# Performance work log

Measured on AMD Instinct MI355X. Metric: run time of the kernel, lower is better.

The kernel has to match this reference:

```python
import jax, jax.numpy as jnp
import numpy as np

DIM = 96; NH = 3; HD = DIM // NH; SCALE = HD ** -0.5
WS = (7, 7, 7); N = WS[0] * WS[1] * WS[2]
SHIFT = (3, 3, 3)  # half window
NL = 2
GRID = (28, 28, 28)
B = 2


def _rel_index():
    wd, wh, ww = WS
    coords = np.stack(np.meshgrid(np.arange(wd), np.arange(wh), np.arange(ww), indexing='ij')).reshape(3, -1)
    rel = (coords[:, :, None] - coords[:, None, :]).transpose(1, 2, 0)  # [N,N,3]
    rel[..., 0] += wd - 1; rel[..., 1] += wh - 1; rel[..., 2] += ww - 1
    rel[..., 0] *= (2 * wh - 1) * (2 * ww - 1); rel[..., 1] *= (2 * ww - 1)
    return rel.sum(-1)  # [N,N]

REL_IDX = _rel_index()


def _window_partition(x):
    b, D, H, W, C = x.shape
    wd, wh, ww = WS
    x = x.reshape(b, D // wd, wd, H // wh, wh, W // ww, ww, C)
    x = x.transpose(0, 1, 3, 5, 2, 4, 6, 7)
    return x.reshape(-1, N, C)


def _window_reverse(win, b, D, H, W):
    wd, wh, ww = WS
    C = win.shape[-1]
    x = win.reshape(b, D // wd, H // wh, W // ww, wd, wh, ww, C)
    x = x.transpose(0, 1, 4, 2, 5, 3, 6, 7)
    return x.reshape(b, D, H, W, C)


def _compute_mask():
    # MONAI compute_mask for the shifted (SW-MSA) block
    D, H, W = GRID; wd, wh, ww = WS; sd, sh, sw = SHIFT
    img = np.zeros((1, D, H, W, 1), np.float32)
    cnt = 0
    for d in (slice(-wd), slice(-wd, -sd), slice(-sd, None)):
        for h in (slice(-wh), slice(-wh, -sh), slice(-sh, None)):
            for w in (slice(-ww), slice(-ww, -sw), slice(-sw, None)):
                img[:, d, h, w, :] = cnt; cnt += 1
    mw = img.reshape(1, D // wd, wd, H // wh, wh, W // ww, ww, 1)
    mw = mw.transpose(0, 1, 3, 5, 2, 4, 6, 7).reshape(-1, N)  # [nw, N]
    am = mw[:, None, :] - mw[:, :, None]
    return np.where(am != 0, np.float32(-100.0), np.float32(0.0))

MASK = jnp.asarray(_compute_mask())  # [nw, N, N]


def _ln(x, g, b):
    mu = x.mean(-1, keepdims=True)
    var = ((x - mu) ** 2).mean(-1, keepdims=True)
    return (x - mu) / jnp.sqrt(var + 1e-5) * g + b


def _block(x, p, shift, mask):
    b, D, H, W, C = x.shape
    h = _ln(x, p['n1g'], p['n1b'])
    if shift is not None:
        h = jnp.roll(h, (-shift[0], -shift[1], -shift[2]), axis=(1, 2, 3))
    xw = _window_partition(h)  # [b*nw, N, C]
    Bn = xw.shape[0]
    qkv = (xw @ p['qkvw'].T + p['qkvb']).reshape(Bn, N, 3, NH, HD).transpose(2, 0, 3, 1, 4)
    q, k, v = qkv[0] * SCALE, qkv[1], qkv[2]
    attn = jnp.einsum('bhnd,bhmd->bhnm', q, k)
    bias = p['rel'][REL_IDX.reshape(-1)].reshape(N, N, NH).transpose(2, 0, 1)
    attn = attn + bias[None]
    if mask is not None:
        nw = mask.shape[0]
        attn = (attn.reshape(Bn // nw, nw, NH, N, N) + mask[None, :, None]).reshape(Bn, NH, N, N)
    attn = jax.nn.softmax(attn, axis=-1)
    out = jnp.einsum('bhnm,bhmd->bhnd', attn, v).transpose(0, 2, 1, 3).reshape(Bn, N, C)
    out = out @ p['projw'].T + p['projb']
    h = _window_reverse(out, b, D, H, W)
    if shift is not None:
        h = jnp.roll(h, shift, axis=(1, 2, 3))
    x = x + h
    m = _ln(x, p['n2g'], p['n2b'])
    m = jax.nn.gelu(m @ p['fc1w'].T + p['fc1b'], approximate=False) @ p['fc2w'].T + p['fc2b']
    return x + m


def setup_inputs() -> dict:
    key = jax.random.key(0)
    ks = jax.random.split(key, 8)
    nbias = (2 * WS[0] - 1) * (2 * WS[1] - 1) * (2 * WS[2] - 1)
    return {
        'x': jax.random.normal(ks[0], (B,) + GRID + (DIM,), jnp.float32),
        'norm1_g': jnp.ones((NL, DIM), jnp.float32),
        'norm1_b': jnp.zeros((NL, DIM), jnp.float32),
        'qkv_w': jax.random.normal(ks[1], (NL, 3 * DIM, DIM), jnp.float32) * 0.02,
        'qkv_b': jnp.zeros((NL, 3 * DIM), jnp.float32),
        'rel_bias': jax.random.normal(ks[2], (NL, nbias, NH), jnp.float32) * 0.02,
        'proj_w': jax.random.normal(ks[3], (NL, DIM, DIM), jnp.float32) * 0.02,
        'proj_b': jnp.zeros((NL, DIM), jnp.float32),
        'norm2_g': jnp.ones((NL, DIM), jnp.float32),
        'norm2_b': jnp.zeros((NL, DIM), jnp.float32),
        'fc1_w': jax.random.normal(ks[4], (NL, 4 * DIM, DIM), jnp.float32) * 0.02,
        'fc1_b': jnp.zeros((NL, 4 * DIM), jnp.float32),
        'fc2_w': jax.random.normal(ks[5], (NL, DIM, 4 * DIM), jnp.float32) * 0.02,
        'fc2_b': jnp.zeros((NL, DIM), jnp.float32),
    }


def reference(x, norm1_g, norm1_b, qkv_w, qkv_b, rel_bias, proj_w, proj_b,
              norm2_g, norm2_b, fc1_w, fc1_b, fc2_w, fc2_b):
    for i in range(NL):
        p = dict(n1g=norm1_g[i], n1b=norm1_b[i], qkvw=qkv_w[i], qkvb=qkv_b[i],
                 rel=rel_bias[i], projw=proj_w[i], projb=proj_b[i],
                 n2g=norm2_g[i], n2b=norm2_b[i], fc1w=fc1_w[i], fc1b=fc1_b[i],
                 fc2w=fc2_w[i], fc2b=fc2_b[i])
        if i % 2 == 0:
            x = _block(x, p, None, None)  # W-MSA (mask is all-zero for shift=0)
        else:
            x = _block(x, p, SHIFT, MASK)  # SW-MSA
    return x
```

## Files before the change

kernel.cpp:

```cpp
#include <hip/hip_runtime.h>
#include <math.h>

#define DIM 96
#define NHD 3
#define HD 32
#define NWT 343
#define NWIN 128
#define TOK 43904
#define NBIAS 2197
#define SCALE 0.17677669529663687f
#define TPAD 352
#define QTS 5632
#define HSZ (22 * QTS)

typedef __attribute__((ext_vector_type(8))) short bf16x8;
typedef __attribute__((ext_vector_type(4))) float f32x4;

__device__ __forceinline__ unsigned short f2b(float f) {
    union { float f; unsigned int u; } x; x.f = f;
    unsigned int r = (x.u + 0x7fffu + ((x.u >> 16) & 1u)) >> 16;
    return (unsigned short)r;
}
__device__ __forceinline__ unsigned int pk2bf(float a, float b) {
    union { float f; unsigned int u; } x, y; x.f = a; y.f = b;
    return ((x.u + 0x8000u) >> 16) | ((y.u + 0x8000u) & 0xffff0000u);
}
__device__ __forceinline__ float lo16(unsigned int u) {
    union { unsigned int u; float f; } x; x.u = u << 16; return x.f;
}
__device__ __forceinline__ float hi16(unsigned int u) {
    union { unsigned int u; float f; } x; x.u = u & 0xffff0000u; return x.f;
}

__global__ void __launch_bounds__(256) k_cvt4(
        const float* __restrict__ s0, const float* __restrict__ s1,
        const float* __restrict__ s2, const float* __restrict__ s3,
        unsigned short* __restrict__ dst) {
    int i = blockIdx.x * 256 + threadIdx.x;
    if (i >= 221184) return;
    const float* src; int off;
    if (i < 55296)       { src = s0; off = i; }
    else if (i < 73728)  { src = s1; off = i - 55296; }
    else if (i < 147456) { src = s2; off = i - 73728; }
    else                 { src = s3; off = i - 147456; }
    dst[i] = f2b(src[off]);
}

__global__ void __launch_bounds__(256) k_bias(
        const float* __restrict__ rel0, const float* __restrict__ rel1,
        unsigned short* __restrict__ bt) {
    int i = blockIdx.x * 256 + threadIdx.x;
    if (i >= 27 * HSZ) return;
    int off = i % QTS;
    int t = i / QTS;
    int qt = t % 22; t /= 22;
    int head = t % 3; int combo = t / 3;
    int j = off & 7, q4i = (off >> 3) & 3, lm = (off >> 5) & 15, pr = off >> 9;
    int q = min(qt * 16 + lm, 342);
    int kcol = pr * 32 + ((j >> 2) << 4) + q4i * 4 + (j & 3);
    float outv;
    if (kcol >= 343) {
        outv = -100000.0f;
    } else {
        int dq = q / 49, hq = (q / 7) % 7, wq = q % 7;
        int dk = kcol / 49, hk = (kcol / 7) % 7, wk = kcol % 7;
        int ridx = (dq - dk + 6) * 169 + (hq - hk + 6) * 13 + (wq - wk + 6);
        const float* rel = (combo == 0) ? rel0 : rel1;
        float b = rel[ridx * 3 + head];
        if (combo > 0) {
            int ty = combo - 1;
            int rqd = (ty & 4) ? 1 + (dq >= 4) : 0;
            int rqh = (ty & 2) ? 1 + (hq >= 4) : 0;
            int rqw = (ty & 1) ? 1 + (wq >= 4) : 0;
            int rkd = (ty & 4) ? 1 + (dk >= 4) : 0;
            int rkh = (ty & 2) ? 1 + (hk >= 4) : 0;
            int rkw = (ty & 1) ? 1 + (wk >= 4) : 0;
            if (rqd != rkd || rqh != rkh || rqw != rkw) b -= 100.0f;
        }
        outv = b;
    }
    bt[i] = f2b(outv);
}

__global__ void __launch_bounds__(256) k_qkv(
        const float* __restrict__ x, const float* __restrict__ g1,
        const float* __restrict__ b1, const unsigned short* __restrict__ W,
        const float* __restrict__ bias, unsigned short* __restrict__ q,
        unsigned short* __restrict__ k, unsigned short* __restrict__ v, int shift) {
    __shared__ __align__(16) unsigned short lns[64][104];
    __shared__ __align__(16) unsigned short wbuf[96][104];
    int wid = threadIdx.x >> 6, lane = threadIdx.x & 63;
    int lm = lane & 15, q4 = lane >> 4;
    int m0 = blockIdx.x * 64 + wid * 16;
    int bwr[4], nnr[4];
    size_t rowoff[4];
    #pragma unroll
    for (int r = 0; r < 4; ++r) {
        int wtok = m0 + q4 * 4 + r;
        int bw = wtok / NWT, n = wtok % NWT;
        bwr[r] = bw; nnr[r] = n;
        int b = bw >> 6, win = bw & 63;
        int wdi = win >> 4, whi = (win >> 2) & 3, wwi = win & 3;
        int d = n / 49, h = (n / 7) % 7, w = n % 7;
        int sd = (wdi * 7 + d + shift) % 28;
        int sh = (whi * 7 + h + shift) % 28;
        int sw = (wwi * 7 + w + shift) % 28;
        rowoff[r] = (((size_t)(b * 28 + sd) * 28 + sh) * 28 + sw) * 96;
    }
    float val[6][4], g1v[6], b1v[6];
    #pragma unroll
    for (int c = 0; c < 6; ++c) {
        int ncol = c * 16 + lm;
        g1v[c] = g1[ncol]; b1v[c] = b1[ncol];
        #pragma unroll
        for (int r = 0; r < 4; ++r) val[c][r] = x[rowoff[r] + ncol];
    }
    #pragma unroll
    for (int r = 0; r < 4; ++r) {
        float s = 0.f, s2 = 0.f;
        #pragma unroll
        for (int c = 0; c < 6; ++c) { s += val[c][r]; s2 += val[c][r] * val[c][r]; }
        #pragma unroll
        for (int off = 8; off > 0; off >>= 1) {
            s  += __shfl_xor(s,  off, 64);
            s2 += __shfl_xor(s2, off, 64);
        }
        float mu = s * (1.0f / 96.0f);
        float rstd = rsqrtf(s2 * (1.0f / 96.0f) - mu * mu + 1e-5f);
        int row = wid * 16 + q4 * 4 + r;
        #pragma unroll
        for (int c = 0; c < 6; ++c)
            lns[row][c * 16 + lm] = f2b((val[c][r] - mu) * rstd * g1v[c] + b1v[c]);
    }
    __syncthreads();
    bf16x8 a1[3];
    #pragma unroll
    for (int ks = 0; ks < 3; ++ks)
        a1[ks] = *((const bf16x8*)&lns[wid * 16 + lm][ks * 32 + q4 * 8]);
    for (int ch = 0; ch < 3; ++ch) {
        __syncthreads();
        const uint4* src = (const uint4*)(W + ch * 96 * 96);
        for (int s = threadIdx.x; s < 1152; s += 256) {
            int row = s / 12, seg = s % 12;
            *((uint4*)&wbuf[row][seg * 8]) = src[s];
        }
        __syncthreads();
        f32x4 acc[6];
        #pragma unroll
        for (int c = 0; c < 6; ++c) acc[c] = (f32x4){0.f, 0.f, 0.f, 0.f};
        #pragma unroll
        for (int ks = 0; ks < 3; ++ks) {
            #pragma unroll
            for (int c = 0; c < 6; ++c) {
                bf16x8 b = *((const bf16x8*)&wbuf[c * 16 + lm][ks * 32 + q4 * 8]);
                acc[c] = __builtin_amdgcn_mfma_f32_16x16x32_bf16(a1[ks], b, acc[c], 0, 0, 0);
            }
        }
        #pragma unroll
        for (int c = 0; c < 6; ++c) {
            int col = c * 16 + lm;
            int head = col >> 5, hd = col & 31;
            float bb = bias[ch * 96 + col];
            #pragma unroll
            for (int r = 0; r < 4; ++r) {
                int wh = bwr[r] * NHD + head;
                float vv = acc[c][r] + bb;
                if (ch == 0)
                    q[(size_t)wh * (TPAD * 32) + nnr[r] * 32 + hd] = f2b(vv * SCALE);
                else if (ch == 1)
                    k[(size_t)wh * (TPAD * 32) + nnr[r] * 32 + hd] = f2b(vv);
                else
                    v[(size_t)wh * (32 * TPAD) + hd * TPAD + nnr[r]] = f2b(vv);
            }
        }
    }
}

__global__ void __launch_bounds__(256) k_attn(
        const unsigned short* __restrict__ q, const unsigned short* __restrict__ k,
        const unsigned short* __restrict__ vT, const unsigned short* __restrict__ bt,
        unsigned short* __restrict__ o, int tmul) {
    __shared__ __align__(16) unsigned short vts[32 * 360];
    __shared__ __align__(16) unsigned short pbuf[4][2][16 * 40];
    int wh = blockIdx.x / 3, third = blockIdx.x % 3;
    int bw = wh / NHD, head = wh % NHD;
    const unsigned int* vsrc = (const unsigned int*)(vT + (size_t)wh * 32 * TPAD);
    unsigned int* vdst = (unsigned int*)vts;
    for (int i = threadIdx.x; i < 32 * 176; i += 256) {
        int row = i / 176, cc = i - row * 176;
        vdst[row * 180 + cc] = vsrc[i];
    }
    __syncthreads();
    int win = bw & 63;
    int wdi = win >> 4, whi = (win >> 2) & 3, wwi = win & 3;
    int type = ((wdi == 3) ? 4 : 0) | ((whi == 3) ? 2 : 0) | ((wwi == 3) ? 1 : 0);
    const unsigned short* bbase = bt + (size_t)type * tmul + (size_t)head * HSZ;
    int wid = threadIdx.x >> 6, lane = threadIdx.x & 63;
    int lm = lane & 15, q4 = lane >> 4;
    int tb = third * 8 + wid * 2;
    if (tb > 21) return;
    bool dual = (tb + 1 <= 21);
    int qtA = tb, qtB = dual ? tb + 1 : tb;
    const unsigned short* qbase = q + (size_t)wh * TPAD * 32;
    const unsigned short* kbase = k + (size_t)wh * TPAD * 32;
    int qtokA = qtA * 16 + lm, qtokB = qtB * 16 + lm;
    bf16x8 qfA = *((const bf16x8*)(qbase + qtokA * 32 + q4 * 8));
    bf16x8 qfB = *((const bf16x8*)(qbase + qtokB * 32 + q4 * 8));
    const unsigned short* bpA = bbase + (size_t)qtA * QTS + lm * 32 + q4 * 8;
    const unsigned short* bpB = bbase + (size_t)qtB * QTS + lm * 32 + q4 * 8;
    f32x4 aA0 = (f32x4){0.f,0.f,0.f,0.f}, aA1 = aA0, aB0 = aA0, aB1 = aA0;
    float dA = 0.f, dB = 0.f;
    unsigned short* pbA = pbuf[wid][0];
    unsigned short* pbB = pbuf[wid][1];
    bf16x8 kf0n = *((const bf16x8*)(kbase + lm * 32 + q4 * 8));
    bf16x8 kf1n = *((const bf16x8*)(kbase + (16 + lm) * 32 + q4 * 8));
    uint4 bAn = *((const uint4*)bpA);
    uint4 bBn = *((const uint4*)bpB);
    for (int pr = 0; pr < 11; ++pr) {
        int kb0 = pr * 32;
        bf16x8 kf0 = kf0n, kf1 = kf1n;
        uint4 uA = bAn, uB = bBn;
        if (pr < 10) {
            int kb1 = kb0 + 32;
            kf0n = *((const bf16x8*)(kbase + (kb1 + lm) * 32 + q4 * 8));
            kf1n = *((const bf16x8*)(kbase + (kb1 + 16 + lm) * 32 + q4 * 8));
            bAn = *((const uint4*)(bpA + (pr + 1) * 512));
            bBn = *((const uint4*)(bpB + (pr + 1) * 512));
        }
        f32x4 z = (f32x4){0.f, 0.f, 0.f, 0.f};
        f32x4 sA0 = __builtin_amdgcn_mfma_f32_16x16x32_bf16(kf0, qfA, z, 0, 0, 0);
        f32x4 sA1 = __builtin_amdgcn_mfma_f32_16x16x32_bf16(kf1, qfA, z, 0, 0, 0);
        f32x4 sB0 = __builtin_amdgcn_mfma_f32_16x16x32_bf16(kf0, qfB, z, 0, 0, 0);
        f32x4 sB1 = __builtin_amdgcn_mfma_f32_16x16x32_bf16(kf1, qfB, z, 0, 0, 0);
        float pA[8], pB[8];
        pA[0] = __expf(sA0[0] + lo16(uA.x)); pA[1] = __expf(sA0[1] + hi16(uA.x));
        pA[2] = __expf(sA0[2] + lo16(uA.y)); pA[3] = __expf(sA0[3] + hi16(uA.y));
        pA[4] = __expf(sA1[0] + lo16(uA.z)); pA[5] = __expf(sA1[1] + hi16(uA.z));
        pA[6] = __expf(sA1[2] + lo16(uA.w)); pA[7] = __expf(sA1[3] + hi16(uA.w));
        pB[0] = __expf(sB0[0] + lo16(uB.x)); pB[1] = __expf(sB0[1] + hi16(uB.x));
        pB[2] = __expf(sB0[2] + lo16(uB.y)); pB[3] = __expf(sB0[3] + hi16(uB.y));
        pB[4] = __expf(sB1[0] + lo16(uB.z)); pB[5] = __expf(sB1[1] + hi16(uB.z));
        pB[6] = __expf(sB1[2] + lo16(uB.w)); pB[7] = __expf(sB1[3] + hi16(uB.w));
        #pragma unroll
        for (int j = 0; j < 8; ++j) { dA += pA[j]; dB += pB[j]; }
        #pragma unroll
        for (int t = 0; t < 2; ++t) {
            *((unsigned int*)(pbA + lm * 40 + t * 16 + q4 * 4)) =
                pk2bf(pA[t * 4 + 0], pA[t * 4 + 1]);
            *((unsigned int*)(pbA + lm * 40 + t * 16 + q4 * 4 + 2)) =
                pk2bf(pA[t * 4 + 2], pA[t * 4 + 3]);
            *((unsigned int*)(pbB + lm * 40 + t * 16 + q4 * 4)) =
                pk2bf(pB[t * 4 + 0], pB[t * 4 + 1]);
            *((unsigned int*)(pbB + lm * 40 + t * 16 + q4 * 4 + 2)) =
                pk2bf(pB[t * 4 + 2], pB[t * 4 + 3]);
        }
        bf16x8 pfA = *((const bf16x8*)(pbA + lm * 40 + q4 * 8));
        bf16x8 pfB = *((const bf16x8*)(pbB + lm * 40 + q4 * 8));
        bf16x8 v0 = *((const bf16x8*)(vts + lm * 360 + kb0 + q4 * 8));
        bf16x8 v1 = *((const bf16x8*)(vts + (16 + lm) * 360 + kb0 + q4 * 8));
        aA0 = __builtin_amdgcn_mfma_f32_16x16x32_bf16(pfA, v0, aA0, 0, 0, 0);
        aA1 = __builtin_amdgcn_mfma_f32_16x16x32_bf16(pfA, v1, aA1, 0, 0, 0);
        aB0 = __builtin_amdgcn_mfma_f32_16x16x32_bf16(pfB, v0, aB0, 0, 0, 0);
        aB1 = __builtin_amdgcn_mfma_f32_16x16x32_bf16(pfB, v1, aB1, 0, 0, 0);
    }
    dA += __shfl_xor(dA, 16, 64); dA += __shfl_xor(dA, 32, 64);
    dB += __shfl_xor(dB, 16, 64); dB += __shfl_xor(dB, 32, 64);
    #pragma unroll
    for (int r = 0; r < 4; ++r) {
        int qrowA = qtA * 16 + q4 * 4 + r;
        if (qrowA < NWT) {
            float inv = 1.0f / __shfl(dA, q4 * 4 + r, 64);
            unsigned short* op = o + (size_t)(bw * NWT + qrowA) * DIM + head * HD;
            op[lm]      = f2b(aA0[r] * inv);
            op[16 + lm] = f2b(aA1[r] * inv);
        }
    }
    if (dual) {
        #pragma unroll
        for (int r = 0; r < 4; ++r) {
            int qrowB = qtB * 16 + q4 * 4 + r;
            if (qrowB < NWT) {
                float inv = 1.0f / __shfl(dB, q4 * 4 + r, 64);
                unsigned short* op = o + (size_t)(bw * NWT + qrowB) * DIM + head * HD;
                op[lm]      = f2b(aB0[r] * inv);
                op[16 + lm] = f2b(aB1[r] * inv);
            }
        }
    }
}

__global__ void __launch_bounds__(256) k_pm(
        const unsigned short* __restrict__ ao, const unsigned short* __restrict__ Wp,
        const float* __restrict__ pbias, const float* __restrict__ xin,
        float* __restrict__ xout,
        const float* __restrict__ g2, const float* __restrict__ b2,
        const unsigned short* __restrict__ w1, const float* __restrict__ bb1,
        const unsigned short* __restrict__ w2, const float* __restrict__ bb2,
        int shift) {
    __shared__ __align__(16) unsigned short lns[64][104];
    __shared__ __align__(16) unsigned short big[18816];
    int wid = threadIdx.x >> 6, lane = threadIdx.x & 63;
    int lm = lane & 15, q4 = lane >> 4;
    int m0 = blockIdx.x * 64 + wid * 16;
    for (int s = threadIdx.x; s < 1152; s += 256) {
        int row = s / 12, seg = s % 12;
        *((uint4*)&big[row * 104 + seg * 8]) = ((const uint4*)Wp)[s];
    }
    const unsigned short* arow = ao + (size_t)(m0 + lm) * 96;
    bf16x8 a1[3];
    #pragma unroll
    for (int ks = 0; ks < 3; ++ks)
        a1[ks] = *((const bf16x8*)(arow + ks * 32 + q4 * 8));
    __syncthreads();
    f32x4 acc[6];
    #pragma unroll
    for (int c = 0; c < 6; ++c) acc[c] = (f32x4){0.f, 0.f, 0.f, 0.f};
    #pragma unroll
    for (int ks = 0; ks < 3; ++ks) {
        #pragma unroll
        for (int c = 0; c < 6; ++c) {
            bf16x8 b = *((const bf16x8*)&big[(c * 16 + lm) * 104 + ks * 32 + q4 * 8]);
            acc[c] = __builtin_amdgcn_mfma_f32_16x16x32_bf16(a1[ks], b, acc[c], 0, 0, 0);
        }
    }
    size_t rowoff[4];
    #pragma unroll
    for (int r = 0; r < 4; ++r) {
        int wtok = m0 + q4 * 4 + r;
        int bw = wtok / NWT, n = wtok % NWT;
        int b = bw >> 6, win = bw & 63;
        int wdi = win >> 4, whi = (win >> 2) & 3, wwi = win & 3;
        int d = n / 49, h = (n / 7) % 7, w = n % 7;
        int sd = (wdi * 7 + d + shift) % 28;
        int sh = (whi * 7 + h + shift) % 28;
        int sw = (wwi * 7 + w + shift) % 28;
        rowoff[r] = (((size_t)(b * 28 + sd) * 28 + sh) * 28 + sw) * 96;
    }
    float val[6][4], g2v[6], b2v[6];
    #pragma unroll
    for (int c = 0; c < 6; ++c) {
        int n = c * 16 + lm;
        float bb = pbias[n];
        g2v[c] = g2[n]; b2v[c] = b2[n];
        #pragma unroll
        for (int r = 0; r < 4; ++r)
            val[c][r] = xin[rowoff[r] + n] + acc[c][r] + bb;
    }
    #pragma unroll
    for (int r = 0; r < 4; ++r) {
        float s = 0.f, s2 = 0.f;
        #pragma unroll
        for (int c = 0; c < 6; ++c) { s += val[c][r]; s2 += val[c][r] * val[c][r]; }
        #pragma unroll
        for (int off = 8; off > 0; off >>= 1) {
            s  += __shfl_xor(s,  off, 64);
            s2 += __shfl_xor(s2, off, 64);
        }
        float mu = s * (1.0f / 96.0f);
        float rstd = rsqrtf(s2 * (1.0f / 96.0f) - mu * mu + 1e-5f);
        int row = wid * 16 + q4 * 4 + r;
        #pragma unroll
        for (int c = 0; c < 6; ++c)
            lns[row][c * 16 + lm] = f2b((val[c][r] - mu) * rstd * g2v[c] + b2v[c]);
    }
    bf16x8 am[3];
    #pragma unroll
    for (int ks = 0; ks < 3; ++ks)
        am[ks] = *((const bf16x8*)&lns[wid * 16 + lm][ks * 32 + q4 * 8]);
    f32x4 acc2[6];
    #pragma unroll
    for (int c = 0; c < 6; ++c) acc2[c] = (f32x4){0.f, 0.f, 0.f, 0.f};
    unsigned short* hid_ = &big[13952 + wid * 1216];
    for (int ch = 0; ch < 6; ++ch) {
        __syncthreads();
        const uint4* src1 = (const uint4*)(w1 + ch * 64 * 96);
        #pragma unroll
        for (int t = 0; t < 3; ++t) {
            int s = threadIdx.x + t * 256;
            int row = s / 12, seg = s % 12;
            *((uint4*)&big[row * 104 + seg * 8]) = src1[s];
        }
        #pragma unroll
        for (int t = 0; t < 3; ++t) {
            int s = threadIdx.x + t * 256;
            int row = s >> 3, seg = s & 7;
            *((uint4*)&big[6656 + row * 76 + seg * 8]) =
                *((const uint4*)(w2 + row * 384 + ch * 64 + seg * 8));
        }
        __syncthreads();
        f32x4 acc1[4];
        #pragma unroll
        for (int t = 0; t < 4; ++t) acc1[t] = (f32x4){0.f, 0.f, 0.f, 0.f};
        #pragma unroll
        for (int ks = 0; ks < 3; ++ks) {
            #pragma unroll
            for (int t = 0; t < 4; ++t) {
                bf16x8 b = *((const bf16x8*)&big[(t * 16 + lm) * 104 + ks * 32 + q4 * 8]);
                acc1[t] = __builtin_amdgcn_mfma_f32_16x16x32_bf16(am[ks], b, acc1[t], 0, 0, 0);
            }
        }
        #pragma unroll
        for (int t = 0; t < 4; ++t) {
            float bb = bb1[ch * 64 + t * 16 + lm];
            #pragma unroll
            for (int r = 0; r < 4; ++r) {
                float v2 = acc1[t][r] + bb;
                float t2 = v2 * v2;
                float m = fmaf(-0.0713548162f, t2, -1.5957691216f);
                float e = __expf(v2 * m);
                float ge = v2 * (1.0f / (1.0f + e));
                hid_[(q4 * 4 + r) * 76 + t * 16 + lm] = f2b(ge);
            }
        }
        #pragma unroll
        for (int ks2 = 0; ks2 < 2; ++ks2) {
            bf16x8 a = *((const bf16x8*)(hid_ + lm * 76 + ks2 * 32 + q4 * 8));
            #pragma unroll
            for (int c = 0; c < 6; ++c) {
                bf16x8 b = *((const bf16x8*)&big[6656 + (c * 16 + lm) * 76 + ks2 * 32 + q4 * 8]);
                acc2[c] = __builtin_amdgcn_mfma_f32_16x16x32_bf16(a, b, acc2[c], 0, 0, 0);
            }
        }
    }
    #pragma unroll
    for (int c = 0; c < 6; ++c) {
        int n = c * 16 + lm;
        float bb = bb2[n];
        #pragma unroll
        for (int r = 0; r < 4; ++r)
            xout[rowoff[r] + n] = val[c][r] + acc2[c][r] + bb;
    }
}

extern "C" void kernel_launch(void* const* d_in, const int* in_sizes, int n_in,
                              void* d_out, int out_size, void* d_ws, size_t ws_size,
                              hipStream_t stream) {
    const float* x     = (const float*)d_in[0];
    const float* n1g   = (const float*)d_in[1];
    const float* n1b   = (const float*)d_in[2];
    const float* qkvw  = (const float*)d_in[3];
    const float* qkvb  = (const float*)d_in[4];
    const float* relb  = (const float*)d_in[5];
    const float* projw = (const float*)d_in[6];
    const float* projb = (const float*)d_in[7];
    const float* n2g   = (const float*)d_in[8];
    const float* n2b   = (const float*)d_in[9];
    const float* fc1w  = (const float*)d_in[10];
    const float* fc1b  = (const float*)d_in[11];
    const float* fc2w  = (const float*)d_in[12];
    const float* fc2b  = (const float*)d_in[13];
    float* out = (float*)d_out;

    const size_t NEL = (size_t)TOK * DIM;
    const size_t QKN = (size_t)NWIN * NHD * TPAD * 32;
    float* buf_x = (float*)d_ws;
    unsigned short* hbuf = (unsigned short*)(buf_x + NEL);
    unsigned short* bq   = hbuf + NEL;
    unsigned short* bk   = bq + QKN;
    unsigned short* bv   = bk + QKN;
    unsigned short* wts  = bv + QKN;
    unsigned short* wq  = wts;
    unsigned short* wp  = wq + 2 * 27648;
    unsigned short* w1  = wp + 2 * 9216;
    unsigned short* w2  = w1 + 2 * 36864;
    unsigned short* btab = wts + 221184;

    k_cvt4<<<(221184 + 255) / 256, 256, 0, stream>>>(qkvw, projw, fc1w, fc2w, wts);
    k_bias<<<(27 * HSZ + 255) / 256, 256, 0, stream>>>(
        relb, relb + NBIAS * NHD, btab);

    for (int L = 0; L < 2; ++L) {
        int shift = (L == 0) ? 0 : 3;
        const float* xin_l = (L == 0) ? x : buf_x;
        float* xfin = (L == 0) ? buf_x : out;
        const unsigned short* btL = (L == 0) ? btab : btab + 3 * HSZ;
        int tmul = (L == 0) ? 0 : 3 * HSZ;

        k_qkv<<<TOK / 64, 256, 0, stream>>>(xin_l, n1g + L * 96, n1b + L * 96,
                                            wq + L * 27648, qkvb + L * 288,
                                            bq, bk, bv, shift);
        k_attn<<<NWIN * NHD * 3, 256, 0, stream>>>(bq, bk, bv, btL, hbuf, tmul);
        k_pm<<<TOK / 64, 256, 0, stream>>>(hbuf, wp + L * 9216, projb + L * 96,
                                           xin_l, xfin,
                                           n2g + L * 96, n2b + L * 96,
                                           w1 + L * 36864, fc1b + L * 384,
                                           w2 + L * 36864, fc2b + L * 96, shift);
    }
}
```

Baseline: 266.4 us.

## Fuse setup kernels, process three query tiles per wave in attention, prefetch MLP weights

Merges the weight-conversion and bias-table kernels into one setup launch. The attention kernel now splits each window-head over two blocks instead of three, with each wave handling three query tiles. This gives more reuse of each loaded K/V tile and stages V fewer times, at the cost of extra register pressure and some duplicated clamped tiles. The MLP kernel prefetches the next chunk's fc1/fc2 weights into registers during compute, hiding global load latency but also raising register use.

```diff
diff --git a/kernel.cpp b/kernel.cpp
--- a/kernel.cpp
+++ b/kernel.cpp
@@ -12,6 +12,7 @@
 #define TPAD 352
 #define QTS 5632
 #define HSZ (22 * QTS)
+#define NWTS 221184
 
 typedef __attribute__((ext_vector_type(8))) short bf16x8;
 typedef __attribute__((ext_vector_type(4))) float f32x4;
@@ -32,25 +33,18 @@
     union { unsigned int u; float f; } x; x.u = u & 0xffff0000u; return x.f;
 }
 
-__global__ void __launch_bounds__(256) k_cvt4(
-        const float* __restrict__ s0, const float* __restrict__ s1,
-        const float* __restrict__ s2, const float* __restrict__ s3,
-        unsigned short* __restrict__ dst) {
-    int i = blockIdx.x * 256 + threadIdx.x;
-    if (i >= 221184) return;
+__device__ __forceinline__ unsigned short cvt_elem(
+        int i, const float* s0, const float* s1, const float* s2, const float* s3) {
     const float* src; int off;
     if (i < 55296)       { src = s0; off = i; }
     else if (i < 73728)  { src = s1; off = i - 55296; }
     else if (i < 147456) { src = s2; off = i - 73728; }
     else                 { src = s3; off = i - 147456; }
-    dst[i] = f2b(src[off]);
-}
-
-__global__ void __launch_bounds__(256) k_bias(
-        const float* __restrict__ rel0, const float* __restrict__ rel1,
-        unsigned short* __restrict__ bt) {
-    int i = blockIdx.x * 256 + threadIdx.x;
-    if (i >= 27 * HSZ) return;
+    return f2b(src[off]);
+}
+
+__device__ __forceinline__ unsigned short bias_elem(
+        int i, const float* rel0, const float* rel1) {
     int off = i % QTS;
     int t = i / QTS;
     int qt = t % 22; t /= 22;
@@ -79,7 +73,18 @@
         }
         outv = b;
     }
-    bt[i] = f2b(outv);
+    return f2b(outv);
+}
+
+__global__ void __launch_bounds__(256) k_setup(
+        const float* __restrict__ qkvw, const float* __restrict__ projw,
+        const float* __restrict__ fc1w, const float* __restrict__ fc2w,
+        const float* __restrict__ rel0, const float* __restrict__ rel1,
+        unsigned short* __restrict__ wts, unsigned short* __restrict__ btab) {
+    int i = blockIdx.x * 256 + threadIdx.x;
+    if (i < NWTS) { wts[i] = cvt_elem(i, qkvw, projw, fc1w, fc2w); return; }
+    int j = i - NWTS;
+    if (j < 27 * HSZ) btab[j] = bias_elem(j, rel0, rel1);
 }
 
 __global__ void __launch_bounds__(256) k_qkv(
@@ -181,8 +186,8 @@
         const unsigned short* __restrict__ vT, const unsigned short* __restrict__ bt,
         unsigned short* __restrict__ o, int tmul) {
     __shared__ __align__(16) unsigned short vts[32 * 360];
-    __shared__ __align__(16) unsigned short pbuf[4][2][16 * 40];
-    int wh = blockIdx.x / 3, third = blockIdx.x % 3;
+    __shared__ __align__(16) unsigned short pbuf[4][3][640];
+    int wh = blockIdx.x >> 1, half = blockIdx.x & 1;
     int bw = wh / NHD, head = wh % NHD;
     const unsigned int* vsrc = (const unsigned int*)(vT + (size_t)wh * 32 * TPAD);
     unsigned int* vdst = (unsigned int*)vts;
@@ -197,93 +202,96 @@
     const unsigned short* bbase = bt + (size_t)type * tmul + (size_t)head * HSZ;
     int wid = threadIdx.x >> 6, lane = threadIdx.x & 63;
     int lm = lane & 15, q4 = lane >> 4;
-    int tb = third * 8 + wid * 2;
-    if (tb > 21) return;
-    bool dual = (tb + 1 <= 21);
-    int qtA = tb, qtB = dual ? tb + 1 : tb;
     const unsigned short* qbase = q + (size_t)wh * TPAD * 32;
     const unsigned short* kbase = k + (size_t)wh * TPAD * 32;
-    int qtokA = qtA * 16 + lm, qtokB = qtB * 16 + lm;
-    bf16x8 qfA = *((const bf16x8*)(qbase + qtokA * 32 + q4 * 8));
-    bf16x8 qfB = *((const bf16x8*)(qbase + qtokB * 32 + q4 * 8));
-    const unsigned short* bpA = bbase + (size_t)qtA * QTS + lm * 32 + q4 * 8;
-    const unsigned short* bpB = bbase + (size_t)qtB * QTS + lm * 32 + q4 * 8;
-    f32x4 aA0 = (f32x4){0.f,0.f,0.f,0.f}, aA1 = aA0, aB0 = aA0, aB1 = aA0;
-    float dA = 0.f, dB = 0.f;
-    unsigned short* pbA = pbuf[wid][0];
-    unsigned short* pbB = pbuf[wid][1];
+    int qt[3];
+    bf16x8 qf[3];
+    const unsigned short* bp[3];
+    f32x4 ac0[3], ac1[3];
+    float dnm[3];
+    #pragma unroll
+    for (int i = 0; i < 3; ++i) {
+        qt[i] = half * 11 + min(wid + 4 * i, 10);
+        qf[i] = *((const bf16x8*)(qbase + (qt[i] * 16 + lm) * 32 + q4 * 8));
+        bp[i] = bbase + (size_t)qt[i] * QTS + lm * 32 + q4 * 8;
+        ac0[i] = (f32x4){0.f, 0.f, 0.f, 0.f};
+        ac1[i] = (f32x4){0.f, 0.f, 0.f, 0.f};
+        dnm[i] = 0.f;
+    }
     bf16x8 kf0n = *((const bf16x8*)(kbase + lm * 32 + q4 * 8));
     bf16x8 kf1n = *((const bf16x8*)(kbase + (16 + lm) * 32 + q4 * 8));
-    uint4 bAn = *((const uint4*)bpA);
-    uint4 bBn = *((const uint4*)bpB);
+    uint4 bn[3];
+    #pragma unroll
+    for (int i = 0; i < 3; ++i) bn[i] = *((const uint4*)bp[i]);
     for (int pr = 0; pr < 11; ++pr) {
         int kb0 = pr * 32;
         bf16x8 kf0 = kf0n, kf1 = kf1n;
-        uint4 uA = bAn, uB = bBn;
+        uint4 u[3];
+        #pragma unroll
+        for (int i = 0; i < 3; ++i) u[i] = bn[i];
         if (pr < 10) {
-            int kb1 = kb0 + 32;
-            kf0n = *((const bf16x8*)(kbase + (kb1 + lm) * 32 + q4 * 8));
-            kf1n = *((const bf16x8*)(kbase + (kb1 + 16 + lm) * 32 + q4 * 8));
-            bAn = *((const uint4*)(bpA + (pr + 1) * 512));
-            bBn = *((const uint4*)(bpB + (pr + 1) * 512));
+            kf0n = *((const bf16x8*)(kbase + (kb0 + 32 + lm) * 32 + q4 * 8));
+            kf1n = *((const bf16x8*)(kbase + (kb0 + 48 + lm) * 32 + q4 * 8));
+            #pragma unroll
+            for (int i = 0; i < 3; ++i)
+                bn[i] = *((const uint4*)(bp[i] + (pr + 1) * 512));
         }
         f32x4 z = (f32x4){0.f, 0.f, 0.f, 0.f};
-        f32x4 sA0 = __builtin_amdgcn_mfma_f32_16x16x32_bf16(kf0, qfA, z, 0, 0, 0);
-        f32x4 sA1 = __builtin_amdgcn_mfma_f32_16x16x32_bf16(kf1, qfA, z, 0, 0, 0);
-        f32x4 sB0 = __builtin_amdgcn_mfma_f32_16x16x32_bf16(kf0, qfB, z, 0, 0, 0);
-        f32x4 sB1 = __builtin_amdgcn_mfma_f32_16x16x32_bf16(kf1, qfB, z, 0, 0, 0);
-        float pA[8], pB[8];
-        pA[0] = __expf(sA0[0] + lo16(uA.x)); pA[1] = __expf(sA0[1] + hi16(uA.x));
-        pA[2] = __expf(sA0[2] + lo16(uA.y)); pA[3] = __expf(sA0[3] + hi16(uA.y));
-        pA[4] = __expf(sA1[0] + lo16(uA.z)); pA[5] = __expf(sA1[1] + hi16(uA.z));
-        pA[6] = __expf(sA1[2] + lo16(uA.w)); pA[7] = __expf(sA1[3] + hi16(uA.w));
-        pB[0] = __expf(sB0[0] + lo16(uB.x)); pB[1] = __expf(sB0[1] + hi16(uB.x));
-        pB[2] = __expf(sB0[2] + lo16(uB.y)); pB[3] = __expf(sB0[3] + hi16(uB.y));
-        pB[4] = __expf(sB1[0] + lo16(uB.z)); pB[5] = __expf(sB1[1] + hi16(uB.z));
-        pB[6] = __expf(sB1[2] + lo16(uB.w)); pB[7] = __expf(sB1[3] + hi16(uB.w));
-        #pragma unroll
-        for (int j = 0; j < 8; ++j) { dA += pA[j]; dB += pB[j]; }
-        #pragma unroll
-        for (int t = 0; t < 2; ++t) {
-            *((unsigned int*)(pbA + lm * 40 + t * 16 + q4 * 4)) =
-                pk2bf(pA[t * 4 + 0], pA[t * 4 + 1]);
-            *((unsigned int*)(pbA + lm * 40 + t * 16 + q4 * 4 + 2)) =
-                pk2bf(pA[t * 4 + 2], pA[t * 4 + 3]);
-            *((unsigned int*)(pbB + lm * 40 + t * 16 + q4 * 4)) =
-                pk2bf(pB[t * 4 + 0], pB[t * 4 + 1]);
-            *((unsigned int*)(pbB + lm * 40 + t * 16 + q4 * 4 + 2)) =
-                pk2bf(pB[t * 4 + 2], pB[t * 4 + 3]);
-        }
-        bf16x8 pfA = *((const bf16x8*)(pbA + lm * 40 + q4 * 8));
-        bf16x8 pfB = *((const bf16x8*)(pbB + lm * 40 + q4 * 8));
+        f32x4 s0[3], s1[3];
+        #pragma unroll
+        for (int i = 0; i < 3; ++i) {
+            s0[i] = __builtin_amdgcn_mfma_f32_16x16x32_bf16(kf0, qf[i], z, 0, 0, 0);
+            s1[i] = __builtin_amdgcn_mfma_f32_16x16x32_bf16(kf1, qf[i], z, 0, 0, 0);
+        }
+        float p[3][8];
+        #pragma unroll
+        for (int i = 0; i < 3; ++i) {
+            p[i][0] = __expf(s0[i][0] + lo16(u[i].x));
+            p[i][1] = __expf(s0[i][1] + hi16(u[i].x));
+            p[i][2] = __expf(s0[i][2] + lo16(u[i].y));
+            p[i][3] = __expf(s0[i][3] + hi16(u[i].y));
+            p[i][4] = __expf(s1[i][0] + lo16(u[i].z));
+            p[i][5] = __expf(s1[i][1] + hi16(u[i].z));
+            p[i][6] = __expf(s1[i][2] + lo16(u[i].w));
+            p[i][7] = __expf(s1[i][3] + hi16(u[i].w));
+            #pragma unroll
+            for (int j = 0; j < 8; ++j) dnm[i] += p[i][j];
+        }
+        #pragma unroll
+        for (int i = 0; i < 3; ++i) {
+            unsigned short* pb = &pbuf[wid][i][0];
+            #pragma unroll
+            for (int t = 0; t < 2; ++t) {
+                *((unsigned int*)(pb + lm * 40 + t * 16 + q4 * 4)) =
+                    pk2bf(p[i][t * 4 + 0], p[i][t * 4 + 1]);
+                *((unsigned int*)(pb + lm * 40 + t * 16 + q4 * 4 + 2)) =
+                    pk2bf(p[i][t * 4 + 2], p[i][t * 4 + 3]);
+            }
+        }
         bf16x8 v0 = *((const bf16x8*)(vts + lm * 360 + kb0 + q4 * 8));
         bf16x8 v1 = *((const bf16x8*)(vts + (16 + lm) * 360 + kb0 + q4 * 8));
-        aA0 = __builtin_amdgcn_mfma_f32_16x16x32_bf16(pfA, v0, aA0, 0, 0, 0);
-        aA1 = __builtin_amdgcn_mfma_f32_16x16x32_bf16(pfA, v1, aA1, 0, 0, 0);
-        aB0 = __builtin_amdgcn_mfma_f32_16x16x32_bf16(pfB, v0, aB0, 0, 0, 0);
-        aB1 = __builtin_amdgcn_mfma_f32_16x16x32_bf16(pfB, v1, aB1, 0, 0, 0);
-    }
-    dA += __shfl_xor(dA, 16, 64); dA += __shfl_xor(dA, 32, 64);
-    dB += __shfl_xor(dB, 16, 64); dB += __shfl_xor(dB, 32, 64);
-    #pragma unroll
-    for (int r = 0; r < 4; ++r) {
-        int qrowA = qtA * 16 + q4 * 4 + r;
-        if (qrowA < NWT) {
-            float inv = 1.0f / __shfl(dA, q4 * 4 + r, 64);
-            unsigned short* op = o + (size_t)(bw * NWT + qrowA) * DIM + head * HD;
-            op[lm]      = f2b(aA0[r] * inv);
-            op[16 + lm] = f2b(aA1[r] * inv);
-        }
-    }
-    if (dual) {
+        #pragma unroll
+        for (int i = 0; i < 3; ++i) {
+            bf16x8 pf = *((const bf16x8*)(&pbuf[wid][i][0] + lm * 40 + q4 * 8));
+            ac0[i] = __builtin_amdgcn_mfma_f32_16x16x32_bf16(pf, v0, ac0[i], 0, 0, 0);
+            ac1[i] = __builtin_amdgcn_mfma_f32_16x16x32_bf16(pf, v1, ac1[i], 0, 0, 0);
+        }
+    }
+    #pragma unroll
+    for (int i = 0; i < 3; ++i) {
+        dnm[i] += __shfl_xor(dnm[i], 16, 64);
+        dnm[i] += __shfl_xor(dnm[i], 32, 64);
+    }
+    #pragma unroll
+    for (int i = 0; i < 3; ++i) {
         #pragma unroll
         for (int r = 0; r < 4; ++r) {
-            int qrowB = qtB * 16 + q4 * 4 + r;
-            if (qrowB < NWT) {
-                float inv = 1.0f / __shfl(dB, q4 * 4 + r, 64);
-                unsigned short* op = o + (size_t)(bw * NWT + qrowB) * DIM + head * HD;
-                op[lm]      = f2b(aB0[r] * inv);
-                op[16 + lm] = f2b(aB1[r] * inv);
+            int qrow = qt[i] * 16 + q4 * 4 + r;
+            if (qrow < NWT) {
+                float inv = 1.0f / __shfl(dnm[i], q4 * 4 + r, 64);
+                unsigned short* op = o + (size_t)(bw * NWT + qrow) * DIM + head * HD;
+                op[lm]      = f2b(ac0[i][r] * inv);
+                op[16 + lm] = f2b(ac1[i][r] * inv);
             }
         }
     }
@@ -302,6 +310,14 @@
     int wid = threadIdx.x >> 6, lane = threadIdx.x & 63;
     int lm = lane & 15, q4 = lane >> 4;
     int m0 = blockIdx.x * 64 + wid * 16;
+    uint4 r1[3], r2[3];
+    #pragma unroll
+    for (int t = 0; t < 3; ++t) {
+        int s = threadIdx.x + t * 256;
+        r1[t] = ((const uint4*)w1)[s];
+        int row = s >> 3, seg = s & 7;
+        r2[t] = *((const uint4*)(w2 + row * 384 + seg * 8));
+    }
     for (int s = threadIdx.x; s < 1152; s += 256) {
         int row = s / 12, seg = s % 12;
         *((uint4*)&big[row * 104 + seg * 8]) = ((const uint4*)Wp)[s];
@@ -373,21 +389,29 @@
     unsigned short* hid_ = &big[13952 + wid * 1216];
     for (int ch = 0; ch < 6; ++ch) {
         __syncthreads();
-        const uint4* src1 = (const uint4*)(w1 + ch * 64 * 96);
         #pragma unroll
         for (int t = 0; t < 3; ++t) {
             int s = threadIdx.x + t * 256;
             int row = s / 12, seg = s % 12;
-            *((uint4*)&big[row * 104 + seg * 8]) = src1[s];
+            *((uint4*)&big[row * 104 + seg * 8]) = r1[t];
         }
         #pragma unroll
         for (int t = 0; t < 3; ++t) {
             int s = threadIdx.x + t * 256;
             int row = s >> 3, seg = s & 7;
-            *((uint4*)&big[6656 + row * 76 + seg * 8]) =
-                *((const uint4*)(w2 + row * 384 + ch * 64 + seg * 8));
+            *((uint4*)&big[6656 + row * 76 + seg * 8]) = r2[t];
         }
         __syncthreads();
+        if (ch < 5) {
+            const uint4* src1 = (const uint4*)(w1 + (ch + 1) * 64 * 96);
+            #pragma unroll
+            for (int t = 0; t < 3; ++t) {
+                int s = threadIdx.x + t * 256;
+                r1[t] = src1[s];
+                int row = s >> 3, seg = s & 7;
+                r2[t] = *((const uint4*)(w2 + row * 384 + (ch + 1) * 64 + seg * 8));
+            }
+        }
         f32x4 acc1[4];
         #pragma unroll
         for (int t = 0; t < 4; ++t) acc1[t] = (f32x4){0.f, 0.f, 0.f, 0.f};
@@ -463,11 +487,11 @@
     unsigned short* wp  = wq + 2 * 27648;
     unsigned short* w1  = wp + 2 * 9216;
     unsigned short* w2  = w1 + 2 * 36864;
-    unsigned short* btab = wts + 221184;
-
-    k_cvt4<<<(221184 + 255) / 256, 256, 0, stream>>>(qkvw, projw, fc1w, fc2w, wts);
-    k_bias<<<(27 * HSZ + 255) / 256, 256, 0, stream>>>(
-        relb, relb + NBIAS * NHD, btab);
+    unsigned short* btab = wts + NWTS;
+
+    int setup_n = NWTS + 27 * HSZ;
+    k_setup<<<(setup_n + 255) / 256, 256, 0, stream>>>(
+        qkvw, projw, fc1w, fc2w, relb, relb + NBIAS * NHD, wts, btab);
 
     for (int L = 0; L < 2; ++L) {
         int shift = (L == 0) ? 0 : 3;
@@ -479,7 +503,7 @@
         k_qkv<<<TOK / 64, 256, 0, stream>>>(xin_l, n1g + L * 96, n1b + L * 96,
                                             wq + L * 27648, qkvb + L * 288,
                                             bq, bk, bv, shift);
-        k_attn<<<NWIN * NHD * 3, 256, 0, stream>>>(bq, bk, bv, btL, hbuf, tmul);
+        k_attn<<<NWIN * NHD * 2, 256, 0, stream>>>(bq, bk, bv, btL, hbuf, tmul);
         k_pm<<<TOK / 64, 256, 0, stream>>>(hbuf, wp + L * 9216, projb + L * 96,
                                            xin_l, xfin,
                                            n2g + L * 96, n2b + L * 96,
```

Result: slower. 290.5 us (+9.1%).
